# Kernel optimization log

Hardware: AMD Instinct MI355X
Metric: run time of the kernel (lower is better)

Reference implementation:

```python
import jax, jax.numpy as jnp
import numpy as np

B, S, H = 1, 2048, 2048
HD, NQ, NKV = 128, 16, 4
FFH = 8192
EPS = 1e-5
ROPE_BASE = 10000.0
SOFTMAX_CAP = 50.0
CLIP_L, CLIP_R = 0.0, 1.0


def setup_inputs() -> dict:
    key = jax.random.key(0)
    ks = jax.random.split(key, 10)
    std = 0.02
    return {
        "x": jax.random.normal(ks[0], (B, S, H), dtype=jnp.float32),
        "attn_norm_w": jax.random.uniform(ks[1], (H,), minval=-1.0, maxval=1.0, dtype=jnp.float32),
        "mlp_norm_w": jax.random.uniform(ks[2], (H,), minval=-1.0, maxval=1.0, dtype=jnp.float32),
        "wq": jax.random.normal(ks[3], (H, NQ * HD), dtype=jnp.float32) * std,
        "wk": jax.random.normal(ks[4], (H, NKV * HD), dtype=jnp.float32) * std,
        "wv": jax.random.normal(ks[5], (H, NKV * HD), dtype=jnp.float32) * std,
        "wo": jax.random.normal(ks[6], (NQ * HD, H), dtype=jnp.float32) * std,
        "w_gate": jax.random.normal(ks[7], (H, FFH), dtype=jnp.float32) * std,
        "w_up": jax.random.normal(ks[8], (H, FFH), dtype=jnp.float32) * std,
        "w_down": jax.random.normal(ks[9], (FFH, H), dtype=jnp.float32) * std,
    }


def _rms_norm(x, w):
    # GroupRMSNorm with group_size=None -> whole hidden dim
    var = jnp.mean(jnp.square(x), axis=-1, keepdims=True)
    return x * jax.lax.rsqrt(var + EPS) * w


def _rope_cos_sin(seq_len, dim):
    inv_freq = 1.0 / (ROPE_BASE ** (jnp.arange(0, dim, 2, dtype=jnp.float32) / dim))
    t = jnp.arange(seq_len, dtype=jnp.float32)
    freqs = jnp.outer(t, inv_freq)                      # [S, dim/2]
    emb = jnp.concatenate([freqs, freqs], axis=-1)      # [S, dim]
    return jnp.cos(emb), jnp.sin(emb)


def _apply_rope(x, cos, sin):
    # x: [B, S, h, d]; rotate-half (LLaMA-style)
    d = x.shape[-1]
    x1, x2 = x[..., : d // 2], x[..., d // 2 :]
    rot = jnp.concatenate([-x2, x1], axis=-1)
    return x * cos[None, :, None, :] + rot * sin[None, :, None, :]


def _qk_norm(x):
    # per-head RMS norm over head_dim (qk_norm_group_size == head_dim), unit weight
    var = jnp.mean(jnp.square(x), axis=-1, keepdims=True)
    return x * jax.lax.rsqrt(var + EPS)


def reference(x, attn_norm_w, mlp_norm_w, wq, wk, wv, wo, w_gate, w_up, w_down):
    # ---- attention sub-layer ----
    h = _rms_norm(x, attn_norm_w)                                     # [B,S,H]
    q = (h @ wq).reshape(B, S, NQ, HD)
    k = (h @ wk).reshape(B, S, NKV, HD)
    v = (h @ wv).reshape(B, S, NKV, HD)

    cos, sin = _rope_cos_sin(S, HD)
    q = _apply_rope(q, cos, sin)
    k = _apply_rope(k, cos, sin)

    q = _qk_norm(q)
    k = _qk_norm(k)

    # GQA: expand kv heads to match q heads
    rep = NQ // NKV
    k = jnp.repeat(k, rep, axis=2)                                    # [B,S,NQ,HD]
    v = jnp.repeat(v, rep, axis=2)

    scale = 1.0 / jnp.sqrt(jnp.float32(HD))
    scores = jnp.einsum("bshd,bthd->bhst", q, k) * scale              # [B,NQ,S,S]
    # softmax cap: cap * tanh(s / cap)
    scores = SOFTMAX_CAP * jnp.tanh(scores / SOFTMAX_CAP)
    causal = jnp.tril(jnp.ones((S, S), dtype=bool))
    scores = jnp.where(causal[None, None], scores, -jnp.inf)
    p = jax.nn.softmax(scores, axis=-1)
    # clip range (l, r): clamp(p * (r - l) + l, 0, 1)
    p = jnp.clip(p * (CLIP_R - CLIP_L) + CLIP_L, 0.0, 1.0)
    o = jnp.einsum("bhst,bthd->bshd", p, v).reshape(B, S, NQ * HD)
    x = x + o @ wo

    # ---- MLP sub-layer (gated SiLU) ----
    h2 = _rms_norm(x, mlp_norm_w)
    mlp_out = (jax.nn.silu(h2 @ w_gate) * (h2 @ w_up)) @ w_down
    return x + mlp_out
```

## Files before the change

kernel.cpp:

```cpp
#include <hip/hip_runtime.h>

typedef __bf16 bf16;
typedef __bf16 bf16x4 __attribute__((ext_vector_type(4)));
typedef __bf16 bf16x8 __attribute__((ext_vector_type(8)));
typedef float f32x4 __attribute__((ext_vector_type(4)));

#define GLP16(gp, lp) __builtin_amdgcn_global_load_lds( \
    (const __attribute__((address_space(1))) void*)(gp), \
    (__attribute__((address_space(3))) void*)(lp), 16, 0, 0)

__device__ __forceinline__ f32x4 mfma16(bf16x8 a, bf16x8 b, f32x4 c) {
    return __builtin_amdgcn_mfma_f32_16x16x32_bf16(a, b, c, 0, 0, 0);
}

__global__ __launch_bounds__(256) void k_rmsnorm(const float* __restrict__ x,
        const float* __restrict__ w, bf16* __restrict__ out) {
    const int H = 2048;
    size_t row = blockIdx.x;
    const float* xr = x + row * H;
    int base = threadIdx.x * 8;
    float4 a = *(const float4*)(xr + base);
    float4 b = *(const float4*)(xr + base + 4);
    float ss = a.x*a.x + a.y*a.y + a.z*a.z + a.w*a.w
             + b.x*b.x + b.y*b.y + b.z*b.z + b.w*b.w;
#pragma unroll
    for (int m = 32; m > 0; m >>= 1) ss += __shfl_xor(ss, m);
    __shared__ float red[4];
    if ((threadIdx.x & 63) == 0) red[threadIdx.x >> 6] = ss;
    __syncthreads();
    float tot = red[0] + red[1] + red[2] + red[3];
    float rs = rsqrtf(tot * (1.0f / H) + 1e-5f);
    float4 wa = *(const float4*)(w + base);
    float4 wb = *(const float4*)(w + base + 4);
    bf16x8 ov;
    ov[0] = (bf16)(a.x * rs * wa.x); ov[1] = (bf16)(a.y * rs * wa.y);
    ov[2] = (bf16)(a.z * rs * wa.z); ov[3] = (bf16)(a.w * rs * wa.w);
    ov[4] = (bf16)(b.x * rs * wb.x); ov[5] = (bf16)(b.y * rs * wb.y);
    ov[6] = (bf16)(b.z * rs * wb.z); ov[7] = (bf16)(b.w * rs * wb.w);
    *(bf16x8*)(out + row * H + base) = ov;
}

__global__ __launch_bounds__(256) void k_convT(const float* __restrict__ W,
        bf16* __restrict__ Wt, int K, int N) {
    __shared__ float t[32][33];
    int k0 = blockIdx.x * 32, n0 = blockIdx.y * 32;
    int tx = threadIdx.x, ty = threadIdx.y;
#pragma unroll
    for (int i = 0; i < 4; i++)
        t[ty + i * 8][tx] = W[(size_t)(k0 + ty + i * 8) * N + n0 + tx];
    __syncthreads();
#pragma unroll
    for (int i = 0; i < 4; i++)
        Wt[(size_t)(n0 + ty + i * 8) * K + k0 + tx] = (bf16)t[tx][ty + i * 8];
}

__global__ __launch_bounds__(256) void k_transpose(const bf16* __restrict__ in,
        bf16* __restrict__ out, int R, int C) {
    __shared__ bf16 t[32][33];
    int r0 = blockIdx.x * 32, c0 = blockIdx.y * 32;
    int tx = threadIdx.x & 31, ty = threadIdx.x >> 5;
#pragma unroll
    for (int i = 0; i < 4; i++)
        t[ty + i * 8][tx] = in[(size_t)(r0 + ty + i * 8) * C + c0 + tx];
    __syncthreads();
#pragma unroll
    for (int i = 0; i < 4; i++)
        out[(size_t)(c0 + ty + i * 8) * R + r0 + tx] = t[tx][ty + i * 8];
}

template<int EPI>
__global__ __launch_bounds__(512, 2) void k_gemm3(const bf16* __restrict__ A,
        const bf16* __restrict__ Bt, void* __restrict__ outp,
        const void* __restrict__ aux, int M, int N, int K, int ksplit) {
    extern __shared__ char lds[];
    const int tid = threadIdx.x, wave = tid >> 6, lane = tid & 63;
    const int lr = lane & 15, kg = lane >> 4;
    const int wm = wave >> 2, wn = wave & 3;
    const int bn = blockIdx.x, bm = blockIdx.y, split = blockIdx.z;
    const int row0 = bm * 256, col0 = bn * 256;
    const int kbeg = split * ksplit;
    const int NT = ksplit >> 5;
    const size_t K2 = (size_t)K * 2;

    size_t offS[2];
#pragma unroll
    for (int s = 0; s < 2; s++) {
        int d = s * 8192 + tid * 16;
        int line = d >> 7, w = d & 127;
        int w2 = w ^ ((line & 7) << 4);
        offS[s] = (size_t)(line * 2 + (w2 >> 6)) * K2 + (w2 & 63);
    }
    const char* Ab = (const char*)A + ((size_t)row0 * K + kbeg) * 2;
    const char* Bb = (const char*)Bt + ((size_t)col0 * K + kbeg) * 2;

    auto stA = [&](int s) {
        const char* src = Ab + (size_t)s * 64;
        char* dst = lds + (s & 3) * 16384 + wave * 1024;
        GLP16(src + offS[0], dst);
        GLP16(src + offS[1], dst + 8192);
    };
    auto stB = [&](int s) {
        const char* src = Bb + (size_t)s * 64;
        char* dst = lds + 65536 + (s & 3) * 16384 + wave * 1024;
        GLP16(src + offS[0], dst);
        GLP16(src + offS[1], dst + 8192);
    };
    auto frag = [&](const char* base, int row) -> bf16x8 {
        int line = row >> 1;
        int pos = (((row & 1) << 6) + (kg << 4)) ^ ((line & 7) << 4);
        return *(const bf16x8*)(base + line * 128 + pos);
    };

    f32x4 acc[8][4];
#pragma unroll
    for (int m = 0; m < 8; m++)
#pragma unroll
        for (int n = 0; n < 4; n++) acc[m][n] = (f32x4){0, 0, 0, 0};

    stA(0); stB(0);
    if (NT > 1) { stA(1); stB(1); }
    if (NT > 2) { stA(2); stB(2); }
    if (NT > 2)      asm volatile("s_waitcnt vmcnt(8)" ::: "memory");
    else if (NT > 1) asm volatile("s_waitcnt vmcnt(4)" ::: "memory");
    else             asm volatile("s_waitcnt vmcnt(0)" ::: "memory");
    __builtin_amdgcn_s_barrier();

    for (int s = 0; s < NT; ++s) {
        const char* As_ = lds + (s & 3) * 16384;
        const char* Bs_ = lds + 65536 + (s & 3) * 16384;
        bf16x8 av[4], bv[4];
#pragma unroll
        for (int m = 0; m < 4; m++) av[m] = frag(As_, wm * 128 + m * 16 + lr);
#pragma unroll
        for (int n = 0; n < 4; n++) bv[n] = frag(Bs_, wn * 64 + n * 16 + lr);
        if (s + 3 < NT) stA(s + 3);
        __builtin_amdgcn_s_barrier();
        asm volatile("s_waitcnt lgkmcnt(0)" ::: "memory");
        __builtin_amdgcn_s_setprio(1);
#pragma unroll
        for (int m = 0; m < 4; m++)
#pragma unroll
            for (int n = 0; n < 4; n++)
                acc[m][n] = mfma16(av[m], bv[n], acc[m][n]);
        __builtin_amdgcn_s_setprio(0);
        __builtin_amdgcn_s_barrier();
        bf16x8 aw[4];
#pragma unroll
        for (int m = 0; m < 4; m++) aw[m] = frag(As_, wm * 128 + (m + 4) * 16 + lr);
        if (s + 3 < NT) stB(s + 3);
        __builtin_amdgcn_s_barrier();
        asm volatile("s_waitcnt lgkmcnt(0)" ::: "memory");
        __builtin_amdgcn_s_setprio(1);
#pragma unroll
        for (int m = 0; m < 4; m++)
#pragma unroll
            for (int n = 0; n < 4; n++)
                acc[m + 4][n] = mfma16(aw[m], bv[n], acc[m + 4][n]);
        __builtin_amdgcn_s_setprio(0);
        if (s + 3 < NT)      asm volatile("s_waitcnt vmcnt(8)" ::: "memory");
        else if (s + 2 < NT) asm volatile("s_waitcnt vmcnt(4)" ::: "memory");
        else if (s + 1 < NT) asm volatile("s_waitcnt vmcnt(0)" ::: "memory");
        __builtin_amdgcn_s_barrier();
    }

#pragma unroll
    for (int m = 0; m < 8; m++)
#pragma unroll
        for (int n = 0; n < 4; n++)
#pragma unroll
            for (int r = 0; r < 4; r++) {
                size_t row = row0 + wm * 128 + m * 16 + kg * 4 + r;
                size_t col = col0 + wn * 64 + n * 16 + lr;
                size_t idx = row * N + col;
                float vv = acc[m][n][r];
                if (EPI == 0) {
                    ((bf16*)outp)[idx] = (bf16)vv;
                } else if (EPI == 2) {
                    float g = (float)((const bf16*)aux)[idx];
                    float sg = g / (1.0f + __expf(-g));
                    ((bf16*)outp)[idx] = (bf16)(sg * vv);
                } else {
                    ((float*)outp)[(size_t)split * M * N + idx] = vv;
                }
            }
}

__global__ __launch_bounds__(256) void k_reduce(const float* __restrict__ parts,
        const float* __restrict__ resid, float* __restrict__ out,
        int ns, size_t n4) {
    size_t i = (size_t)blockIdx.x * 256 + threadIdx.x;
    if (i >= n4) return;
    float4 acc = ((const float4*)resid)[i];
    for (int s = 0; s < ns; s++) {
        float4 p = ((const float4*)(parts + (size_t)s * n4 * 4))[i];
        acc.x += p.x; acc.y += p.y; acc.z += p.z; acc.w += p.w;
    }
    ((float4*)out)[i] = acc;
}

__global__ __launch_bounds__(256) void k_reduce_rms(const float* __restrict__ parts,
        const float* __restrict__ resid, const float* __restrict__ w,
        float* __restrict__ x2, bf16* __restrict__ hb, int ns) {
    const int H = 2048;
    size_t row = blockIdx.x;
    int base = threadIdx.x * 8;
    const float* rr = resid + row * H + base;
    float4 a = *(const float4*)rr;
    float4 b = *(const float4*)(rr + 4);
    for (int s = 0; s < ns; s++) {
        const float* pp = parts + (size_t)s * H * 2048 + row * H + base;
        float4 pa = *(const float4*)pp;
        float4 pb = *(const float4*)(pp + 4);
        a.x += pa.x; a.y += pa.y; a.z += pa.z; a.w += pa.w;
        b.x += pb.x; b.y += pb.y; b.z += pb.z; b.w += pb.w;
    }
    *(float4*)(x2 + row * H + base) = a;
    *(float4*)(x2 + row * H + base + 4) = b;
    float ss = a.x*a.x + a.y*a.y + a.z*a.z + a.w*a.w
             + b.x*b.x + b.y*b.y + b.z*b.z + b.w*b.w;
#pragma unroll
    for (int m = 32; m > 0; m >>= 1) ss += __shfl_xor(ss, m);
    __shared__ float red[4];
    if ((threadIdx.x & 63) == 0) red[threadIdx.x >> 6] = ss;
    __syncthreads();
    float tot = red[0] + red[1] + red[2] + red[3];
    float rs = rsqrtf(tot * (1.0f / H) + 1e-5f);
    float4 wa = *(const float4*)(w + base);
    float4 wb = *(const float4*)(w + base + 4);
    bf16x8 ov;
    ov[0] = (bf16)(a.x * rs * wa.x); ov[1] = (bf16)(a.y * rs * wa.y);
    ov[2] = (bf16)(a.z * rs * wa.z); ov[3] = (bf16)(a.w * rs * wa.w);
    ov[4] = (bf16)(b.x * rs * wb.x); ov[5] = (bf16)(b.y * rs * wb.y);
    ov[6] = (bf16)(b.z * rs * wb.z); ov[7] = (bf16)(b.w * rs * wb.w);
    *(bf16x8*)(hb + row * H + base) = ov;
}

__global__ __launch_bounds__(256) void k_qkvfin(const float* __restrict__ parts,
        bf16* __restrict__ qb, bf16* __restrict__ kb, bf16* __restrict__ vb) {
    int s = blockIdx.x;
    int col = blockIdx.y * 1024 + threadIdx.x * 4;
    const float* p0 = parts + (size_t)s * 3072 + col;
    const float* p1 = p0 + (size_t)2048 * 3072;
    float4 a = *(const float4*)p0;
    float4 b = *(const float4*)p1;
    a.x += b.x; a.y += b.y; a.z += b.z; a.w += b.w;
    bf16x4 o;
    o[0] = (bf16)a.x; o[1] = (bf16)a.y; o[2] = (bf16)a.z; o[3] = (bf16)a.w;
    if (col < 2048)      *(bf16x4*)(qb + (size_t)s * 2048 + col) = o;
    else if (col < 2560) *(bf16x4*)(kb + (size_t)s * 512 + col - 2048) = o;
    else                 *(bf16x4*)(vb + (size_t)s * 512 + col - 2560) = o;
}

__global__ __launch_bounds__(64) void k_rope(bf16* __restrict__ q,
        bf16* __restrict__ k) {
    int s = blockIdx.x, hid = blockIdx.y, lane = threadIdx.x;
    bf16* p;
    if (hid < 16) p = q + (size_t)s * 2048 + hid * 128;
    else          p = k + (size_t)s * 512 + (hid - 16) * 128;
    float x1 = (float)p[lane], x2 = (float)p[lane + 64];
    float f = exp2f((float)lane * -0.2076205059304601f);
    float sn, cs;
    sincosf((float)s * f, &sn, &cs);
    float o1 = x1 * cs - x2 * sn;
    float o2 = x2 * cs + x1 * sn;
    float ss = o1 * o1 + o2 * o2;
#pragma unroll
    for (int m = 32; m > 0; m >>= 1) ss += __shfl_xor(ss, m);
    float rs = rsqrtf(ss * (1.0f / 128.0f) + 1e-5f);
    p[lane] = (bf16)(o1 * rs);
    p[lane + 64] = (bf16)(o2 * rs);
}

__global__ __launch_bounds__(256) void k_attn(const bf16* __restrict__ qg,
        const bf16* __restrict__ kgl, const bf16* __restrict__ vtg,
        bf16* __restrict__ og) {
    extern __shared__ char alds[];
    int pi = blockIdx.x, h = blockIdx.y, kvh = h >> 2;
    int tid = threadIdx.x, wave = tid >> 6, lane = tid & 63;
    int lr = lane & 15, kgrp = lane >> 4;

    int rowQ[4], colQ[4], rowV[4], colV[4];
#pragma unroll
    for (int j = 0; j < 4; j++) {
        int p = j * 4096 + wave * 1024 + lane * 16;
        int ps = p ^ (((p >> 8) & 7) << 4);
        rowQ[j] = ps >> 8; colQ[j] = ps & 255;
        int pv = p ^ (((p >> 7) & 7) << 4);
        rowV[j] = pv >> 7; colV[j] = pv & 127;
    }

    const float C1 = 0.08838834764831845f / 50.0f;
    const float L2E50 = 72.13475204444817f;

#pragma unroll 1
    for (int half = 0; half < 2; ++half) {
        int qt = half ? (31 - pi) : pi;
        int nt = qt + 1;

#pragma unroll
        for (int j = 0; j < 4; j++)
            GLP16((const char*)qg + (size_t)(qt * 64 + rowQ[j]) * 4096 + h * 256 + colQ[j],
                  alds + j * 4096 + wave * 1024);
        for (int t = 0; t < 2 && t < nt; t++) {
#pragma unroll
            for (int j = 0; j < 4; j++)
                GLP16((const char*)kgl + (size_t)(t * 64 + rowQ[j]) * 1024 + kvh * 256 + colQ[j],
                      alds + 16384 + t * 16384 + j * 4096 + wave * 1024);
#pragma unroll
            for (int j = 0; j < 4; j++)
                GLP16((const char*)vtg + (size_t)(kvh * 128 + rowV[j]) * 4096 + t * 128 + colV[j],
                      alds + 49152 + t * 16384 + j * 4096 + wave * 1024);
        }
        if (nt > 1) asm volatile("s_waitcnt vmcnt(8)" ::: "memory");
        else        asm volatile("s_waitcnt vmcnt(0)" ::: "memory");
        __builtin_amdgcn_s_barrier();

        bf16x8 qf[4];
#pragma unroll
        for (int c = 0; c < 4; c++) {
            int b = (wave * 16 + lr) * 256 + c * 64 + kgrp * 16;
            qf[c] = *(const bf16x8*)(alds + (b ^ (((b >> 8) & 7) << 4)));
        }
        f32x4 accO[8];
#pragma unroll
        for (int n = 0; n < 8; n++) accO[n] = (f32x4){0, 0, 0, 0};
        float lsum[4] = {0, 0, 0, 0};
        int qrow = qt * 64 + wave * 16 + kgrp * 4;

        for (int kt = 0; kt < nt; kt++) {
            int buf = kt & 1;
            const char* Kb = alds + 16384 + buf * 16384;
            const char* Vb = alds + 49152 + buf * 16384;
            char* Pb = alds + 81920;
#pragma unroll
            for (int j = 0; j < 4; j++) {
                f32x4 s = {0, 0, 0, 0};
#pragma unroll
                for (int c = 0; c < 4; c++) {
                    int b = (j * 16 + lr) * 256 + c * 64 + kgrp * 16;
                    bf16x8 kf = *(const bf16x8*)(Kb + (b ^ (((b >> 8) & 7) << 4)));
                    s = mfma16(qf[c], kf, s);
                }
                int key = kt * 64 + j * 16 + lr;
#pragma unroll
                for (int r = 0; r < 4; r++) {
                    float y = s[r] * C1;
                    float y2 = y * y;
                    float u = fmaf(y2, 0.13333333f, -0.33333333f);
                    u = fmaf(y2, u, 1.0f);
                    float t5 = y * u;
                    float pe = fmaf(t5, L2E50, -L2E50);
                    float pv = (key <= qrow + r) ? exp2f(pe) : 0.0f;
                    lsum[r] += pv;
                    int wb = (wave * 16 + kgrp * 4 + r) * 128 + (j * 16 + lr) * 2;
                    *(bf16*)(Pb + (wb ^ (((wb >> 7) & 7) << 4))) = (bf16)pv;
                }
            }
            bf16x8 pf[2];
#pragma unroll
            for (int ks2 = 0; ks2 < 2; ks2++) {
                int b = (wave * 16 + lr) * 128 + ks2 * 64 + kgrp * 16;
                pf[ks2] = *(const bf16x8*)(Pb + (b ^ (((b >> 7) & 7) << 4)));
            }
#pragma unroll
            for (int n = 0; n < 8; n++)
#pragma unroll
                for (int ks2 = 0; ks2 < 2; ks2++) {
                    int b = (n * 16 + lr) * 128 + ks2 * 64 + kgrp * 16;
                    bf16x8 vf = *(const bf16x8*)(Vb + (b ^ (((b >> 7) & 7) << 4)));
                    accO[n] = mfma16(pf[ks2], vf, accO[n]);
                }
            __builtin_amdgcn_s_barrier();
            bool more = (kt + 2 < nt);
            if (more) {
                int t = kt + 2;
#pragma unroll
                for (int j = 0; j < 4; j++)
                    GLP16((const char*)kgl + (size_t)(t * 64 + rowQ[j]) * 1024 + kvh * 256 + colQ[j],
                          alds + 16384 + buf * 16384 + j * 4096 + wave * 1024);
#pragma unroll
                for (int j = 0; j < 4; j++)
                    GLP16((const char*)vtg + (size_t)(kvh * 128 + rowV[j]) * 4096 + t * 128 + colV[j],
                          alds + 49152 + buf * 16384 + j * 4096 + wave * 1024);
            }
            if (kt + 1 < nt) {
                if (more) asm volatile("s_waitcnt vmcnt(8)" ::: "memory");
                else      asm volatile("s_waitcnt vmcnt(0)" ::: "memory");
                __builtin_amdgcn_s_barrier();
            }
        }
#pragma unroll
        for (int r = 0; r < 4; r++) {
            float t = lsum[r];
            t += __shfl_xor(t, 1); t += __shfl_xor(t, 2);
            t += __shfl_xor(t, 4); t += __shfl_xor(t, 8);
            lsum[r] = t;
        }
#pragma unroll
        for (int n = 0; n < 8; n++)
#pragma unroll
            for (int r = 0; r < 4; r++) {
                size_t row = qt * 64 + wave * 16 + kgrp * 4 + r;
                og[row * 2048 + h * 128 + n * 16 + lr] = (bf16)(accO[n][r] / lsum[r]);
            }
    }
}

extern "C" void kernel_launch(void* const* d_in, const int* in_sizes, int n_in,
                              void* d_out, int out_size, void* d_ws, size_t ws_size,
                              hipStream_t stream) {
    const float* x      = (const float*)d_in[0];
    const float* attn_w = (const float*)d_in[1];
    const float* mlp_w  = (const float*)d_in[2];
    const float* wq     = (const float*)d_in[3];
    const float* wk     = (const float*)d_in[4];
    const float* wv     = (const float*)d_in[5];
    const float* wo     = (const float*)d_in[6];
    const float* wgate  = (const float*)d_in[7];
    const float* wup    = (const float*)d_in[8];
    const float* wdown  = (const float*)d_in[9];
    float* out = (float*)d_out;
    char* ws = (char*)d_ws;

    const size_t MB = 1024 * 1024;
    bf16* W1  = (bf16*)(ws + 0);
    bf16* W2  = (bf16*)(ws + 32 * MB);
    bf16* W3  = (bf16*)(ws + 64 * MB);
    bf16* hb  = (bf16*)(ws + 96 * MB);
    bf16* qb  = (bf16*)(ws + 104 * MB);
    bf16* kb  = (bf16*)(ws + 112 * MB);
    bf16* vb  = (bf16*)(ws + 114 * MB);
    bf16* ob  = (bf16*)(ws + 116 * MB);
    float* x2 = (float*)(ws + 124 * MB);
    bf16* gb  = (bf16*)(ws + 140 * MB);
    bf16* vt  = (bf16*)(ws + 0);
    float* parts = (float*)(ws + 0);
    float* partsq = (float*)(ws + 116 * MB);

    const int LDS3 = 131072;
    hipFuncSetAttribute((const void*)&k_gemm3<0>,
        hipFuncAttributeMaxDynamicSharedMemorySize, LDS3);
    hipFuncSetAttribute((const void*)&k_gemm3<2>,
        hipFuncAttributeMaxDynamicSharedMemorySize, LDS3);
    hipFuncSetAttribute((const void*)&k_gemm3<3>,
        hipFuncAttributeMaxDynamicSharedMemorySize, LDS3);
    const int LDSA = 90112;
    hipFuncSetAttribute((const void*)&k_attn,
        hipFuncAttributeMaxDynamicSharedMemorySize, LDSA);

    dim3 cb(32, 8);
    const size_t n4 = (size_t)2048 * 2048 / 4;

    k_rmsnorm<<<2048, 256, 0, stream>>>(x, attn_w, hb);
    k_convT<<<dim3(64, 64), cb, 0, stream>>>(wq, W1, 2048, 2048);
    k_convT<<<dim3(64, 16), cb, 0, stream>>>(wk, W1 + 4194304, 2048, 512);
    k_convT<<<dim3(64, 16), cb, 0, stream>>>(wv, W1 + 5242880, 2048, 512);
    k_gemm3<3><<<dim3(12, 8, 2), 512, LDS3, stream>>>(hb, W1, partsq, nullptr,
                                                      2048, 3072, 2048, 1024);
    k_qkvfin<<<dim3(2048, 3), 256, 0, stream>>>(partsq, qb, kb, vb);
    k_transpose<<<dim3(64, 16), 256, 0, stream>>>(vb, vt, 2048, 512);
    k_rope<<<dim3(2048, 20), 64, 0, stream>>>(qb, kb);
    k_attn<<<dim3(16, 16), 256, LDSA, stream>>>(qb, kb, vt, ob);
    k_convT<<<dim3(64, 64), cb, 0, stream>>>(wo, W2, 2048, 2048);
    k_gemm3<3><<<dim3(8, 8, 2), 512, LDS3, stream>>>(ob, W2, parts, nullptr,
                                                     2048, 2048, 2048, 1024);
    k_reduce_rms<<<2048, 256, 0, stream>>>(parts, x, mlp_w, x2, hb, 2);
    k_convT<<<dim3(64, 256), cb, 0, stream>>>(wgate, W1, 2048, 8192);
    k_gemm3<0><<<dim3(32, 8, 1), 512, LDS3, stream>>>(hb, W1, gb, nullptr,
                                                      2048, 8192, 2048, 2048);
    k_convT<<<dim3(64, 256), cb, 0, stream>>>(wup, W2, 2048, 8192);
    k_gemm3<2><<<dim3(32, 8, 1), 512, LDS3, stream>>>(hb, W2, gb, gb,
                                                      2048, 8192, 2048, 2048);
    k_convT<<<dim3(256, 64), cb, 0, stream>>>(wdown, W3, 8192, 2048);
    k_gemm3<3><<<dim3(8, 8, 4), 512, LDS3, stream>>>(gb, W3, parts, nullptr,
                                                     2048, 2048, 8192, 2048);
    k_reduce<<<4096, 256, 0, stream>>>(parts, x2, out, 4, n4);
}
```

Before: 489.7 us.

## Restructure GEMM mainloop into 64-wide K tiles with quadrant-phased double buffering

The bf16 GEMM now stages 64-element K tiles (128-byte rows) in two double-buffered halves instead of 32-element tiles in a 4-deep ring. Each K tile is computed as four 128x128 quadrant phases, each guarded by barriers and sched_barriers. Global-to-LDS loads for the next tile's quadrants are interleaved between these MFMA phases, in the style of ping-pong scheduling. The LDS swizzle and the per-wave output mapping change to match. The aim is better overlap of memory and MFMA work with fewer barriers per K element, at the cost of a shallower prefetch depth. It also assumes NT is even.

Result: faster. 473.6 us (-3.3%).

```diff
diff --git a/kernel.cpp b/kernel.cpp
--- a/kernel.cpp
+++ b/kernel.cpp
@@ -69,7 +69,7 @@
 }
 
 template<int EPI>
-__global__ __launch_bounds__(512, 2) void k_gemm3(const bf16* __restrict__ A,
+__global__ __launch_bounds__(512, 2) void k_gemm4(const bf16* __restrict__ A,
         const bf16* __restrict__ Bt, void* __restrict__ outp,
         const void* __restrict__ aux, int M, int N, int K, int ksplit) {
     extern __shared__ char lds[];
@@ -79,100 +79,148 @@
     const int bn = blockIdx.x, bm = blockIdx.y, split = blockIdx.z;
     const int row0 = bm * 256, col0 = bn * 256;
     const int kbeg = split * ksplit;
-    const int NT = ksplit >> 5;
+    const int NT = ksplit >> 6;
     const size_t K2 = (size_t)K * 2;
-
-    size_t offS[2];
+    const int xorm = (lr & 7) << 4;
+
+    char* const A0 = lds;
+    char* const A1 = lds + 32768;
+    char* const B0 = lds + 65536;
+    char* const B1 = lds + 98304;
+
+    size_t soff[2];
 #pragma unroll
     for (int s = 0; s < 2; s++) {
         int d = s * 8192 + tid * 16;
-        int line = d >> 7, w = d & 127;
-        int w2 = w ^ ((line & 7) << 4);
-        offS[s] = (size_t)(line * 2 + (w2 >> 6)) * K2 + (w2 & 63);
+        int rh = d >> 7, c = d & 127;
+        soff[s] = (size_t)rh * K2 + (c ^ ((rh & 7) << 4));
     }
     const char* Ab = (const char*)A + ((size_t)row0 * K + kbeg) * 2;
     const char* Bb = (const char*)Bt + ((size_t)col0 * K + kbeg) * 2;
 
-    auto stA = [&](int s) {
-        const char* src = Ab + (size_t)s * 64;
-        char* dst = lds + (s & 3) * 16384 + wave * 1024;
-        GLP16(src + offS[0], dst);
-        GLP16(src + offS[1], dst + 8192);
+    auto stA = [&](int t, int mh) {
+        const char* src = Ab + (size_t)(mh * 128) * K2 + (size_t)t * 128;
+        char* dst = lds + (t & 1) * 32768 + mh * 16384 + wave * 1024;
+        GLP16(src + soff[0], dst);
+        GLP16(src + soff[1], dst + 8192);
     };
-    auto stB = [&](int s) {
-        const char* src = Bb + (size_t)s * 64;
-        char* dst = lds + 65536 + (s & 3) * 16384 + wave * 1024;
-        GLP16(src + offS[0], dst);
-        GLP16(src + offS[1], dst + 8192);
+    auto stB = [&](int t, int nh) {
+        const char* src = Bb + (size_t)(nh * 128) * K2 + (size_t)t * 128;
+        char* dst = lds + 65536 + (t & 1) * 32768 + nh * 16384 + wave * 1024;
+        GLP16(src + soff[0], dst);
+        GLP16(src + soff[1], dst + 8192);
     };
-    auto frag = [&](const char* base, int row) -> bf16x8 {
-        int line = row >> 1;
-        int pos = (((row & 1) << 6) + (kg << 4)) ^ ((line & 7) << 4);
-        return *(const bf16x8*)(base + line * 128 + pos);
+
+    f32x4 acc[8][4];
+#pragma unroll
+    for (int m = 0; m < 8; m++)
+#pragma unroll
+        for (int n = 0; n < 4; n++) acc[m][n] = (f32x4){0, 0, 0, 0};
+
+    bf16x8 a[8], c0[4], c1[4];
+    auto rdA = [&](const char* base, int mh) {
+#pragma unroll
+        for (int mi = 0; mi < 4; mi++)
+#pragma unroll
+            for (int kk = 0; kk < 2; kk++) {
+                int rh = wm * 64 + mi * 16 + lr;
+                int c = (kk * 64 + kg * 16) ^ xorm;
+                a[mi * 2 + kk] = *(const bf16x8*)(base + mh * 16384 + rh * 128 + c);
+            }
     };
-
-    f32x4 acc[8][4];
-#pragma unroll
-    for (int m = 0; m < 8; m++)
-#pragma unroll
-        for (int n = 0; n < 4; n++) acc[m][n] = (f32x4){0, 0, 0, 0};
-
-    stA(0); stB(0);
-    if (NT > 1) { stA(1); stB(1); }
-    if (NT > 2) { stA(2); stB(2); }
-    if (NT > 2)      asm volatile("s_waitcnt vmcnt(8)" ::: "memory");
-    else if (NT > 1) asm volatile("s_waitcnt vmcnt(4)" ::: "memory");
-    else             asm volatile("s_waitcnt vmcnt(0)" ::: "memory");
+    auto rdB = [&](const char* base, int nh, bf16x8 (&b)[4]) {
+#pragma unroll
+        for (int nj = 0; nj < 2; nj++)
+#pragma unroll
+            for (int kk = 0; kk < 2; kk++) {
+                int rh = wn * 32 + nj * 16 + lr;
+                int c = (kk * 64 + kg * 16) ^ xorm;
+                b[nj * 2 + kk] = *(const bf16x8*)(base + nh * 16384 + rh * 128 + c);
+            }
+    };
+    auto mm = [&](int mh, int nh, bf16x8 (&b)[4]) {
+#pragma unroll
+        for (int mi = 0; mi < 4; mi++)
+#pragma unroll
+            for (int nj = 0; nj < 2; nj++)
+#pragma unroll
+                for (int kk = 0; kk < 2; kk++)
+                    acc[mh * 4 + mi][nh * 2 + nj] =
+                        mfma16(a[mi * 2 + kk], b[nj * 2 + kk],
+                               acc[mh * 4 + mi][nh * 2 + nj]);
+    };
+
+#define SYNCMM \
+    __builtin_amdgcn_sched_barrier(0); \
+    __builtin_amdgcn_s_barrier(); \
+    asm volatile("s_waitcnt lgkmcnt(0)" ::: "memory"); \
+    __builtin_amdgcn_sched_barrier(0); \
+    __builtin_amdgcn_s_setprio(1);
+#define ENDPH \
+    __builtin_amdgcn_s_setprio(0); \
+    __builtin_amdgcn_sched_barrier(0); \
     __builtin_amdgcn_s_barrier();
 
-    for (int s = 0; s < NT; ++s) {
-        const char* As_ = lds + (s & 3) * 16384;
-        const char* Bs_ = lds + 65536 + (s & 3) * 16384;
-        bf16x8 av[4], bv[4];
-#pragma unroll
-        for (int m = 0; m < 4; m++) av[m] = frag(As_, wm * 128 + m * 16 + lr);
-#pragma unroll
-        for (int n = 0; n < 4; n++) bv[n] = frag(Bs_, wn * 64 + n * 16 + lr);
-        if (s + 3 < NT) stA(s + 3);
+    stA(0, 0); stB(0, 0); stB(0, 1); stA(0, 1);
+    stA(1, 0); stB(1, 0); stB(1, 1);
+    asm volatile("s_waitcnt vmcnt(6)" ::: "memory");
+    __builtin_amdgcn_s_barrier();
+
+    const int NIT = NT >> 1;
+    for (int it = 0; it < NIT; ++it) {
+        const int t = it * 2;
+        const bool more = (t + 2 < NT);
+        rdA(A0, 0); rdB(B0, 0, c0);
+        stA(t + 1, 1);
+        SYNCMM; mm(0, 0, c0); ENDPH;
+        rdB(B0, 1, c1);
+        if (more) stA(t + 2, 0);
+        SYNCMM; mm(0, 1, c1); ENDPH;
+        rdA(A0, 1);
+        if (more) stB(t + 2, 0);
+        SYNCMM; mm(1, 1, c1); ENDPH;
+        if (more) stB(t + 2, 1);
+        __builtin_amdgcn_sched_barrier(0);
         __builtin_amdgcn_s_barrier();
-        asm volatile("s_waitcnt lgkmcnt(0)" ::: "memory");
         __builtin_amdgcn_s_setprio(1);
-#pragma unroll
-        for (int m = 0; m < 4; m++)
-#pragma unroll
-            for (int n = 0; n < 4; n++)
-                acc[m][n] = mfma16(av[m], bv[n], acc[m][n]);
+        mm(1, 0, c0);
         __builtin_amdgcn_s_setprio(0);
+        if (more) asm volatile("s_waitcnt vmcnt(6)" ::: "memory");
+        else      asm volatile("s_waitcnt vmcnt(0)" ::: "memory");
+        __builtin_amdgcn_sched_barrier(0);
         __builtin_amdgcn_s_barrier();
-        bf16x8 aw[4];
-#pragma unroll
-        for (int m = 0; m < 4; m++) aw[m] = frag(As_, wm * 128 + (m + 4) * 16 + lr);
-        if (s + 3 < NT) stB(s + 3);
+        rdA(A1, 0); rdB(B1, 0, c0);
+        if (more) stA(t + 2, 1);
+        SYNCMM; mm(0, 0, c0); ENDPH;
+        rdB(B1, 1, c1);
+        if (t + 3 < NT) stA(t + 3, 0);
+        SYNCMM; mm(0, 1, c1); ENDPH;
+        rdA(A1, 1);
+        if (t + 3 < NT) stB(t + 3, 0);
+        SYNCMM; mm(1, 1, c1); ENDPH;
+        if (t + 3 < NT) stB(t + 3, 1);
+        __builtin_amdgcn_sched_barrier(0);
         __builtin_amdgcn_s_barrier();
-        asm volatile("s_waitcnt lgkmcnt(0)" ::: "memory");
         __builtin_amdgcn_s_setprio(1);
-#pragma unroll
-        for (int m = 0; m < 4; m++)
-#pragma unroll
-            for (int n = 0; n < 4; n++)
-                acc[m + 4][n] = mfma16(aw[m], bv[n], acc[m + 4][n]);
+        mm(1, 0, c0);
         __builtin_amdgcn_s_setprio(0);
-        if (s + 3 < NT)      asm volatile("s_waitcnt vmcnt(8)" ::: "memory");
-        else if (s + 2 < NT) asm volatile("s_waitcnt vmcnt(4)" ::: "memory");
-        else if (s + 1 < NT) asm volatile("s_waitcnt vmcnt(0)" ::: "memory");
+        if (more) asm volatile("s_waitcnt vmcnt(6)" ::: "memory");
+        __builtin_amdgcn_sched_barrier(0);
         __builtin_amdgcn_s_barrier();
     }
-
-#pragma unroll
-    for (int m = 0; m < 8; m++)
-#pragma unroll
-        for (int n = 0; n < 4; n++)
+#undef SYNCMM
+#undef ENDPH
+
+#pragma unroll
+    for (int mi = 0; mi < 8; mi++)
+#pragma unroll
+        for (int ni = 0; ni < 4; ni++)
 #pragma unroll
             for (int r = 0; r < 4; r++) {
-                size_t row = row0 + wm * 128 + m * 16 + kg * 4 + r;
-                size_t col = col0 + wn * 64 + n * 16 + lr;
+                size_t row = row0 + (mi >> 2) * 128 + wm * 64 + (mi & 3) * 16 + kg * 4 + r;
+                size_t col = col0 + (ni >> 1) * 128 + wn * 32 + (ni & 1) * 16 + lr;
                 size_t idx = row * N + col;
-                float vv = acc[m][n][r];
+                float vv = acc[mi][ni][r];
                 if (EPI == 0) {
                     ((bf16*)outp)[idx] = (bf16)vv;
                 } else if (EPI == 2) {
@@ -437,13 +485,13 @@
     float* parts = (float*)(ws + 0);
     float* partsq = (float*)(ws + 116 * MB);
 
-    const int LDS3 = 131072;
-    hipFuncSetAttribute((const void*)&k_gemm3<0>,
-        hipFuncAttributeMaxDynamicSharedMemorySize, LDS3);
-    hipFuncSetAttribute((const void*)&k_gemm3<2>,
-        hipFuncAttributeMaxDynamicSharedMemorySize, LDS3);
-    hipFuncSetAttribute((const void*)&k_gemm3<3>,
-        hipFuncAttributeMaxDynamicSharedMemorySize, LDS3);
+    const int LDS4 = 131072;
+    hipFuncSetAttribute((const void*)&k_gemm4<0>,
+        hipFuncAttributeMaxDynamicSharedMemorySize, LDS4);
+    hipFuncSetAttribute((const void*)&k_gemm4<2>,
+        hipFuncAttributeMaxDynamicSharedMemorySize, LDS4);
+    hipFuncSetAttribute((const void*)&k_gemm4<3>,
+        hipFuncAttributeMaxDynamicSharedMemorySize, LDS4);
     const int LDSA = 90112;
     hipFuncSetAttribute((const void*)&k_attn,
         hipFuncAttributeMaxDynamicSharedMemorySize, LDSA);
@@ -455,24 +503,24 @@
     k_convT<<<dim3(64, 64), cb, 0, stream>>>(wq, W1, 2048, 2048);
     k_convT<<<dim3(64, 16), cb, 0, stream>>>(wk, W1 + 4194304, 2048, 512);
     k_convT<<<dim3(64, 16), cb, 0, stream>>>(wv, W1 + 5242880, 2048, 512);
-    k_gemm3<3><<<dim3(12, 8, 2), 512, LDS3, stream>>>(hb, W1, partsq, nullptr,
+    k_gemm4<3><<<dim3(12, 8, 2), 512, LDS4, stream>>>(hb, W1, partsq, nullptr,
                                                       2048, 3072, 2048, 1024);
     k_qkvfin<<<dim3(2048, 3), 256, 0, stream>>>(partsq, qb, kb, vb);
     k_transpose<<<dim3(64, 16), 256, 0, stream>>>(vb, vt, 2048, 512);
     k_rope<<<dim3(2048, 20), 64, 0, stream>>>(qb, kb);
     k_attn<<<dim3(16, 16), 256, LDSA, stream>>>(qb, kb, vt, ob);
     k_convT<<<dim3(64, 64), cb, 0, stream>>>(wo, W2, 2048, 2048);
-    k_gemm3<3><<<dim3(8, 8, 2), 512, LDS3, stream>>>(ob, W2, parts, nullptr,
+    k_gemm4<3><<<dim3(8, 8, 2), 512, LDS4, stream>>>(ob, W2, parts, nullptr,
                                                      2048, 2048, 2048, 1024);
     k_reduce_rms<<<2048, 256, 0, stream>>>(parts, x, mlp_w, x2, hb, 2);
     k_convT<<<dim3(64, 256), cb, 0, stream>>>(wgate, W1, 2048, 8192);
-    k_gemm3<0><<<dim3(32, 8, 1), 512, LDS3, stream>>>(hb, W1, gb, nullptr,
+    k_gemm4<0><<<dim3(32, 8, 1), 512, LDS4, stream>>>(hb, W1, gb, nullptr,
                                                       2048, 8192, 2048, 2048);
     k_convT<<<dim3(64, 256), cb, 0, stream>>>(wup, W2, 2048, 8192);
-    k_gemm3<2><<<dim3(32, 8, 1), 512, LDS3, stream>>>(hb, W2, gb, gb,
+    k_gemm4<2><<<dim3(32, 8, 1), 512, LDS4, stream>>>(hb, W2, gb, gb,
                                                       2048, 8192, 2048, 2048);
     k_convT<<<dim3(256, 64), cb, 0, stream>>>(wdown, W3, 8192, 2048);
-    k_gemm3<3><<<dim3(8, 8, 4), 512, LDS3, stream>>>(gb, W3, parts, nullptr,
+    k_gemm4<3><<<dim3(8, 8, 4), 512, LDS4, stream>>>(gb, W3, parts, nullptr,
                                                      2048, 2048, 8192, 2048);
     k_reduce<<<4096, 256, 0, stream>>>(parts, x2, out, 4, n4);
 }
```
